# Performance work log

Measured on AMD Instinct MI355X. Metric: run time of the kernel, lower is better.

Reference implementation:

```python
import jax, jax.numpy as jnp
import numpy as np

E = 131072   # total messages
N = 8192     # dim_size (num nodes)
D = 256      # input_dim == hidden_dim (forced by h + m add)


def setup_inputs() -> dict:
    key = jax.random.key(0)
    k1, k2, k3, k4, k5 = jax.random.split(key, 5)
    msg = jax.random.normal(k1, (E, D), dtype=jnp.float32)
    index = jax.random.randint(k2, (E,), 0, N)
    t = jax.random.uniform(k3, (E,), dtype=jnp.float32)
    # torch.nn.Linear(D, D) params (kaiming-uniform-ish scale)
    W = jax.random.normal(k4, (D, D), dtype=jnp.float32) / np.sqrt(D)
    b = (jax.random.normal(k5, (D,), dtype=jnp.float32) * 0.01)
    return {"msg": msg, "index": index, "t": t, "dim_size": N, "W": W, "b": b}


def reference(msg, index, t, dim_size, W, b):
    # Original: for each node, sort its messages by t, then run the linear
    # recurrence h <- W @ (m + h) + b starting from h = 0; nodes with no
    # messages keep h = 0. Vectorized: one global stable sort by (index, t),
    # then a single segmented lax.scan with reset at segment boundaries.
    num_msgs, d = msg.shape
    order = jnp.lexsort((t, index))          # primary key: index, secondary: t
    m_sorted = msg[order]                     # [E, d]
    seg = index[order]                        # [E]

    def step(carry, inp):
        h, prev = carry
        m, s = inp
        h_in = jnp.where(s == prev, h, jnp.zeros_like(h))  # reset at new segment
        h_new = (m + h_in) @ W.T + b
        return (h_new, s), h_new

    init = (jnp.zeros((d,), msg.dtype), jnp.asarray(-1, seg.dtype))
    _, ys = jax.lax.scan(step, init, (m_sorted, seg))      # ys: [E, d]

    # final hidden per node = h at the last message of its segment
    pos = jnp.arange(num_msgs)
    last = jax.ops.segment_max(pos, seg, num_segments=dim_size)
    counts = jax.ops.segment_sum(jnp.ones((num_msgs,), jnp.int32), seg,
                                 num_segments=dim_size)
    gathered = ys[jnp.clip(last, 0, num_msgs - 1)]          # [N, d]
    hidden = jnp.where((counts > 0)[:, None], gathered, jnp.zeros_like(gathered))
    return hidden
```

## Files before the change

### kernel.cpp

```cpp
#include <hip/hip_runtime.h>
#include <hip/hip_bf16.h>

#define E_MSGS 131072
#define N_NODES 8192
#define D_DIM 256
#define XA_STRIDE 264

typedef __bf16 bf16x8 __attribute__((ext_vector_type(8)));
typedef float f32x4 __attribute__((ext_vector_type(4)));

#define BAR() asm volatile("s_waitcnt lgkmcnt(0)\n\ts_barrier" ::: "memory")


__global__ void k_count(const int* __restrict__ index, int* __restrict__ counts) {
    int e = blockIdx.x * blockDim.x + threadIdx.x;
    if (e < E_MSGS) atomicAdd(&counts[index[e]], 1);
}

__global__ void k_prep(const int* __restrict__ counts, int* __restrict__ offsets,
                       int* __restrict__ perm) {
    __shared__ int partial[256];
    __shared__ int hist[256];
    __shared__ int hscan[256];
    __shared__ int hcur[256];
    int tid = threadIdx.x;
    hist[tid] = 0;
    __syncthreads();

    int base = tid * 32;
    int local[32];
    int sum = 0;
#pragma unroll
    for (int i = 0; i < 32; i++) {
        local[i] = sum;
        int c = counts[base + i];
        sum += c;
        atomicAdd(&hist[min(c, 255)], 1);
    }
    partial[tid] = sum;
    __syncthreads();
    for (int off = 1; off < 256; off <<= 1) {
        int v = (tid >= off) ? partial[tid - off] : 0;
        __syncthreads();
        partial[tid] += v;
        __syncthreads();
    }
    int basesum = (tid > 0) ? partial[tid - 1] : 0;
#pragma unroll
    for (int i = 0; i < 32; i++) offsets[base + i] = basesum + local[i];
    if (tid == 255) offsets[N_NODES] = partial[255];

    hscan[tid] = hist[255 - tid];
    __syncthreads();
    for (int off = 1; off < 256; off <<= 1) {
        int v = (tid >= off) ? hscan[tid - off] : 0;
        __syncthreads();
        hscan[tid] += v;
        __syncthreads();
    }
    hcur[tid] = hscan[255 - tid] - hist[tid];
    __syncthreads();
#pragma unroll
    for (int i = 0; i < 32; i++) {
        int n = base + i;
        int c = min(counts[n], 255);
        int pos = atomicAdd(&hcur[c], 1);
        perm[pos] = n;
    }
}

__global__ void k_scatter(const int* __restrict__ index, const int* __restrict__ offsets,
                          int* __restrict__ cursors, int* __restrict__ bucket) {
    int e = blockIdx.x * blockDim.x + threadIdx.x;
    if (e < E_MSGS) {
        int n = index[e];
        int p = offsets[n] + atomicAdd(&cursors[n], 1);
        bucket[p] = e;
    }
}

__global__ void k_sortseg(const float* __restrict__ t, const int* __restrict__ offsets,
                          const int* __restrict__ bucket, int* __restrict__ sorted_id) {
    int wid = (blockIdx.x * 256 + threadIdx.x) >> 6;
    int ln = threadIdx.x & 63;
    int beg = offsets[wid], end = offsets[wid + 1];
    int cnt = end - beg;
    int e = 0; float tv = 0.f;
    if (ln < cnt) { e = bucket[beg + ln]; tv = t[e]; }
    int rank = 0;
    for (int j = 0; j < cnt; j++) {
        float tj = __shfl(tv, j);
        int ej = __shfl(e, j);
        rank += (tj < tv) || (tj == tv && ej < e);
    }
    if (ln < cnt) sorted_id[beg + rank] = e;
}


__launch_bounds__(256, 2)
__global__ void k_gru(const float* __restrict__ msg, const float* __restrict__ W,
                      const float* __restrict__ b, const int* __restrict__ offsets,
                      const int* __restrict__ sorted_id, const int* __restrict__ perm,
                      float* __restrict__ out) {
    __shared__ __bf16 xA[2][16 * XA_STRIDE];

    int tid  = threadIdx.x;
    int wave = tid >> 6;
    int lane = tid & 63;
    int q    = lane >> 4;
    int l    = lane & 15;
    int node0 = blockIdx.x * 16;

    bf16x8 wf[8][4];
#pragma unroll
    for (int t4 = 0; t4 < 4; t4++) {
        const float* wr = W + (64 * wave + 16 * t4 + l) * D_DIM;
#pragma unroll
        for (int c = 0; c < 8; c++) {
            int k0 = 32 * c + 8 * q;
            float4 w0 = *(const float4*)(wr + k0);
            float4 w1 = *(const float4*)(wr + k0 + 4);
            bf16x8 f;
            f[0] = (__bf16)w0.x; f[1] = (__bf16)w0.y; f[2] = (__bf16)w0.z; f[3] = (__bf16)w0.w;
            f[4] = (__bf16)w1.x; f[5] = (__bf16)w1.y; f[6] = (__bf16)w1.z; f[7] = (__bf16)w1.w;
            wf[c][t4] = f;
        }
    }
    float bias[4];
#pragma unroll
    for (int t4 = 0; t4 < 4; t4++) bias[t4] = b[64 * wave + 16 * t4 + l];

    int nodeC[4], off4[4], cnt4[4];
#pragma unroll
    for (int r = 0; r < 4; r++) {
        int n = perm[node0 + 4 * q + r];
        nodeC[r] = n;
        off4[r] = offsets[n];
        cnt4[r] = offsets[n + 1] - off4[r];
    }
    int nfirst = perm[node0];
    int S = offsets[nfirst + 1] - offsets[nfirst];

    float h[4][4];
#pragma unroll
    for (int t4 = 0; t4 < 4; t4++)
#pragma unroll
        for (int r = 0; r < 4; r++) h[t4][r] = 0.f;

    float mvA[4][4], mvB[4][4];
    int sidp[4];
#pragma unroll
    for (int r = 0; r < 4; r++) {
        int sid0 = sorted_id[min(off4[r], E_MSGS - 1)];
        int sid1 = sorted_id[min(off4[r] + 1, E_MSGS - 1)];
        const float* m0 = msg + (long)sid0 * D_DIM;
        const float* m1 = msg + (long)sid1 * D_DIM;
#pragma unroll
        for (int t4 = 0; t4 < 4; t4++) {
            int col = 64 * wave + 16 * t4 + l;
            xA[0][(4 * q + r) * XA_STRIDE + col] = (__bf16)m0[col];
            mvA[r][t4] = m1[col];
        }
        sidp[r] = sorted_id[min(off4[r] + 2, E_MSGS - 1)];
    }
    BAR();

    auto step = [&](int s, float (&cur)[4][4], float (&nxt)[4][4]) {
#pragma unroll
        for (int r = 0; r < 4; r++) {
            const float* mrow = msg + (long)sidp[r] * D_DIM;
#pragma unroll
            for (int t4 = 0; t4 < 4; t4++) nxt[r][t4] = mrow[64 * wave + 16 * t4 + l];
        }
#pragma unroll
        for (int r = 0; r < 4; r++)
            sidp[r] = sorted_id[min(off4[r] + s + 3, E_MSGS - 1)];

        const __bf16* buf = xA[s & 1];
        f32x4 acc[4];
#pragma unroll
        for (int t4 = 0; t4 < 4; t4++) acc[t4] = (f32x4){0.f, 0.f, 0.f, 0.f};
#pragma unroll
        for (int c = 0; c < 8; c++) {
            bf16x8 a = *(const bf16x8*)(buf + l * XA_STRIDE + 32 * c + 8 * q);
#pragma unroll
            for (int t4 = 0; t4 < 4; t4++)
                acc[t4] = __builtin_amdgcn_mfma_f32_16x16x32_bf16(a, wf[c][t4], acc[t4], 0, 0, 0);
        }

        __bf16* nbuf = xA[(s + 1) & 1];
#pragma unroll
        for (int t4 = 0; t4 < 4; t4++) {
#pragma unroll
            for (int r = 0; r < 4; r++) {
                float hn = acc[t4][r] + bias[t4];
                bool valid = s < cnt4[r];
                h[t4][r] = valid ? hn : h[t4][r];
                nbuf[(4 * q + r) * XA_STRIDE + 64 * wave + 16 * t4 + l] =
                    (__bf16)(h[t4][r] + cur[r][t4]);
            }
        }
        BAR();
    };

    int s = 0;
    while (s < S) {
        step(s, mvA, mvB);
        s++;
        if (s >= S) break;
        step(s, mvB, mvA);
        s++;
    }

#pragma unroll
    for (int t4 = 0; t4 < 4; t4++)
#pragma unroll
        for (int r = 0; r < 4; r++)
            out[(long)nodeC[r] * D_DIM + 64 * wave + 16 * t4 + l] = h[t4][r];
}


extern "C" void kernel_launch(void* const* d_in, const int* in_sizes, int n_in,
                              void* d_out, int out_size, void* d_ws, size_t ws_size,
                              hipStream_t stream) {
    const float* msg   = (const float*)d_in[0];
    const int*   index = (const int*)d_in[1];
    const float* t     = (const float*)d_in[2];
    const float* W     = (const float*)d_in[4];
    const float* b     = (const float*)d_in[5];
    float* out = (float*)d_out;

    int* ws = (int*)d_ws;
    int* counts    = ws;
    int* cursors   = ws + 8192;
    int* offsets   = ws + 16384;
    int* perm      = ws + 24584;
    int* bucket    = ws + 32776;
    int* sorted_id = ws + 163848;

    hipMemsetAsync(counts, 0, 16384 * sizeof(int), stream);

    k_count<<<E_MSGS / 256, 256, 0, stream>>>(index, counts);
    k_prep<<<1, 256, 0, stream>>>(counts, offsets, perm);
    k_scatter<<<E_MSGS / 256, 256, 0, stream>>>(index, offsets, cursors, bucket);
    k_sortseg<<<N_NODES * 64 / 256, 256, 0, stream>>>(t, offsets, bucket, sorted_id);
    k_gru<<<N_NODES / 16, 256, 0, stream>>>(msg, W, b, offsets, sorted_id, perm, out);
}
```

Baseline: 256.7 us.

## Fuse per-node time sort into GRU kernel and drop degree-sorted node permutation

The per-segment timestamp sort moves into the recurrence kernel. Each block ranks its 16 nodes' messages with wave shuffles into a shared-memory id table, which removes the separate sort kernel and its global sorted_id round trip. The single-block prefix scan is rewritten as a 1024-thread shuffle scan that also zeroes the scatter cursors, so the memset shrinks. Nodes are now processed in natural order instead of the count-sorted permutation, which drops the histogram work. The cost is that each block runs for the longest segment among its 16 nodes, and segments are capped at 64 messages.

```diff
diff --git a/kernel.cpp b/kernel.cpp
--- a/kernel.cpp
+++ b/kernel.cpp
@@ -17,56 +17,42 @@
     if (e < E_MSGS) atomicAdd(&counts[index[e]], 1);
 }
 
-__global__ void k_prep(const int* __restrict__ counts, int* __restrict__ offsets,
-                       int* __restrict__ perm) {
-    __shared__ int partial[256];
-    __shared__ int hist[256];
-    __shared__ int hscan[256];
-    __shared__ int hcur[256];
-    int tid = threadIdx.x;
-    hist[tid] = 0;
+__global__ void k_scan(const int* __restrict__ counts, int* __restrict__ offsets,
+                       int* __restrict__ cursors) {
+    __shared__ int wsum[16], wpre[16];
+    int tid = threadIdx.x, lane = tid & 63, wave = tid >> 6;
+    int base = tid * 8;
+    int4 c0 = *(const int4*)(counts + base);
+    int4 c1 = *(const int4*)(counts + base + 4);
+    int v[8] = {c0.x, c0.y, c0.z, c0.w, c1.x, c1.y, c1.z, c1.w};
+    int loc[8], sum = 0;
+#pragma unroll
+    for (int i = 0; i < 8; i++) { loc[i] = sum; sum += v[i]; }
+    int incl = sum;
+#pragma unroll
+    for (int d = 1; d < 64; d <<= 1) {
+        int u = __shfl_up(incl, d);
+        if (lane >= d) incl += u;
+    }
+    if (lane == 63) wsum[wave] = incl;
     __syncthreads();
-
-    int base = tid * 32;
-    int local[32];
-    int sum = 0;
-#pragma unroll
-    for (int i = 0; i < 32; i++) {
-        local[i] = sum;
-        int c = counts[base + i];
-        sum += c;
-        atomicAdd(&hist[min(c, 255)], 1);
-    }
-    partial[tid] = sum;
+    if (tid < 16) {
+        int w = wsum[tid], p = w;
+#pragma unroll
+        for (int d = 1; d < 16; d <<= 1) {
+            int u = __shfl_up(p, d);
+            if (tid >= d) p += u;
+        }
+        wpre[tid] = p - w;
+    }
     __syncthreads();
-    for (int off = 1; off < 256; off <<= 1) {
-        int v = (tid >= off) ? partial[tid - off] : 0;
-        __syncthreads();
-        partial[tid] += v;
-        __syncthreads();
-    }
-    int basesum = (tid > 0) ? partial[tid - 1] : 0;
-#pragma unroll
-    for (int i = 0; i < 32; i++) offsets[base + i] = basesum + local[i];
-    if (tid == 255) offsets[N_NODES] = partial[255];
-
-    hscan[tid] = hist[255 - tid];
-    __syncthreads();
-    for (int off = 1; off < 256; off <<= 1) {
-        int v = (tid >= off) ? hscan[tid - off] : 0;
-        __syncthreads();
-        hscan[tid] += v;
-        __syncthreads();
-    }
-    hcur[tid] = hscan[255 - tid] - hist[tid];
-    __syncthreads();
-#pragma unroll
-    for (int i = 0; i < 32; i++) {
-        int n = base + i;
-        int c = min(counts[n], 255);
-        int pos = atomicAdd(&hcur[c], 1);
-        perm[pos] = n;
-    }
+    int ebase = wpre[wave] + incl - sum;
+#pragma unroll
+    for (int i = 0; i < 8; i++) offsets[base + i] = ebase + loc[i];
+    int4 z = {0, 0, 0, 0};
+    *(int4*)(cursors + base) = z;
+    *(int4*)(cursors + base + 4) = z;
+    if (tid == 0) offsets[N_NODES] = E_MSGS;
 }
 
 __global__ void k_scatter(const int* __restrict__ index, const int* __restrict__ offsets,
@@ -79,36 +65,52 @@
     }
 }
 
-__global__ void k_sortseg(const float* __restrict__ t, const int* __restrict__ offsets,
-                          const int* __restrict__ bucket, int* __restrict__ sorted_id) {
-    int wid = (blockIdx.x * 256 + threadIdx.x) >> 6;
-    int ln = threadIdx.x & 63;
-    int beg = offsets[wid], end = offsets[wid + 1];
-    int cnt = end - beg;
-    int e = 0; float tv = 0.f;
-    if (ln < cnt) { e = bucket[beg + ln]; tv = t[e]; }
-    int rank = 0;
-    for (int j = 0; j < cnt; j++) {
-        float tj = __shfl(tv, j);
-        int ej = __shfl(e, j);
-        rank += (tj < tv) || (tj == tv && ej < e);
-    }
-    if (ln < cnt) sorted_id[beg + rank] = e;
-}
-
+
+#define GRU_STEP(SS, CUR, NXT)                                                 \
+    {                                                                          \
+        _Pragma("unroll") for (int r = 0; r < 4; r++) {                        \
+            const float* mrow = msg + (long)sidR[r] * D_DIM;                   \
+            _Pragma("unroll") for (int t4 = 0; t4 < 4; t4++)                   \
+                NXT[r][t4] = mrow[64 * wave + 16 * t4 + l];                     \
+        }                                                                      \
+        {                                                                      \
+            int row = (SS) + 3 < 64 ? (SS) + 3 : 63;                           \
+            int4 sr = *(const int4*)&sid[row][4 * q];                          \
+            sidR[0] = sr.x; sidR[1] = sr.y; sidR[2] = sr.z; sidR[3] = sr.w;    \
+        }                                                                      \
+        const __bf16* buf = xA[(SS) & 1];                                      \
+        f32x4 acc[4];                                                          \
+        _Pragma("unroll") for (int t4 = 0; t4 < 4; t4++)                       \
+            acc[t4] = (f32x4){0.f, 0.f, 0.f, 0.f};                             \
+        _Pragma("unroll") for (int c = 0; c < 8; c++) {                        \
+            bf16x8 a = *(const bf16x8*)(buf + l * XA_STRIDE + 32 * c + 8 * q); \
+            _Pragma("unroll") for (int t4 = 0; t4 < 4; t4++)                   \
+                acc[t4] = __builtin_amdgcn_mfma_f32_16x16x32_bf16(             \
+                    a, wf[c][t4], acc[t4], 0, 0, 0);                           \
+        }                                                                      \
+        __bf16* nbuf = xA[((SS) + 1) & 1];                                     \
+        _Pragma("unroll") for (int t4 = 0; t4 < 4; t4++) {                     \
+            _Pragma("unroll") for (int r = 0; r < 4; r++) {                    \
+                float hn = acc[t4][r] + bias[t4];                              \
+                bool valid = (SS) < cnt4[r];                                   \
+                h[t4][r] = valid ? hn : h[t4][r];                              \
+                nbuf[(4 * q + r) * XA_STRIDE + 64 * wave + 16 * t4 + l] =      \
+                    (__bf16)(h[t4][r] + CUR[r][t4]);                           \
+            }                                                                  \
+        }                                                                      \
+        BAR();                                                                 \
+    }
 
 __launch_bounds__(256, 2)
-__global__ void k_gru(const float* __restrict__ msg, const float* __restrict__ W,
+__global__ void k_gru(const float* __restrict__ msg, const float* __restrict__ t,
+                      const int* __restrict__ bucket, const float* __restrict__ W,
                       const float* __restrict__ b, const int* __restrict__ offsets,
-                      const int* __restrict__ sorted_id, const int* __restrict__ perm,
                       float* __restrict__ out) {
     __shared__ __bf16 xA[2][16 * XA_STRIDE];
-
-    int tid  = threadIdx.x;
-    int wave = tid >> 6;
-    int lane = tid & 63;
-    int q    = lane >> 4;
-    int l    = lane & 15;
+    __shared__ int sid[64][16];
+
+    int tid = threadIdx.x;
+    int wave = tid >> 6, lane = tid & 63, q = lane >> 4, l = lane & 15;
     int node0 = blockIdx.x * 16;
 
     bf16x8 wf[8][4];
@@ -130,16 +132,33 @@
 #pragma unroll
     for (int t4 = 0; t4 < 4; t4++) bias[t4] = b[64 * wave + 16 * t4 + l];
 
-    int nodeC[4], off4[4], cnt4[4];
+    int off4[4], cnt4[4];
 #pragma unroll
     for (int r = 0; r < 4; r++) {
-        int n = perm[node0 + 4 * q + r];
-        nodeC[r] = n;
-        off4[r] = offsets[n];
-        cnt4[r] = offsets[n + 1] - off4[r];
-    }
-    int nfirst = perm[node0];
-    int S = offsets[nfirst + 1] - offsets[nfirst];
+        off4[r] = offsets[node0 + 4 * q + r];
+        cnt4[r] = offsets[node0 + 4 * q + r + 1] - off4[r];
+    }
+    int mc = max(max(cnt4[0], cnt4[1]), max(cnt4[2], cnt4[3]));
+    mc = max(mc, __shfl_xor(mc, 16));
+    mc = max(mc, __shfl_xor(mc, 32));
+    int S = mc;
+
+    for (int i = 0; i < 4; i++) {
+        int j = 4 * wave + i;
+        int beg = offsets[node0 + j];
+        int cnt = min(offsets[node0 + j + 1] - beg, 64);
+        sid[lane][j] = 0;
+        int e = 0; float tv = 0.f;
+        if (lane < cnt) { e = bucket[beg + lane]; tv = t[e]; }
+        int rank = 0;
+        for (int j2 = 0; j2 < cnt; j2++) {
+            float tj = __shfl(tv, j2);
+            int ej = __shfl(e, j2);
+            rank += (tj < tv) || (tj == tv && ej < e);
+        }
+        if (lane < cnt) sid[rank][j] = e;
+    }
+    BAR();
 
     float h[4][4];
 #pragma unroll
@@ -148,75 +167,38 @@
         for (int r = 0; r < 4; r++) h[t4][r] = 0.f;
 
     float mvA[4][4], mvB[4][4];
-    int sidp[4];
+    int sidR[4];
+    int4 sr0 = *(const int4*)&sid[0][4 * q];
+    int4 sr1 = *(const int4*)&sid[1][4 * q];
+    int4 sr2 = *(const int4*)&sid[2][4 * q];
+    int s0[4] = {sr0.x, sr0.y, sr0.z, sr0.w};
+    int s1[4] = {sr1.x, sr1.y, sr1.z, sr1.w};
+    sidR[0] = sr2.x; sidR[1] = sr2.y; sidR[2] = sr2.z; sidR[3] = sr2.w;
 #pragma unroll
     for (int r = 0; r < 4; r++) {
-        int sid0 = sorted_id[min(off4[r], E_MSGS - 1)];
-        int sid1 = sorted_id[min(off4[r] + 1, E_MSGS - 1)];
-        const float* m0 = msg + (long)sid0 * D_DIM;
-        const float* m1 = msg + (long)sid1 * D_DIM;
+        const float* m0 = msg + (long)s0[r] * D_DIM;
+        const float* m1 = msg + (long)s1[r] * D_DIM;
 #pragma unroll
         for (int t4 = 0; t4 < 4; t4++) {
             int col = 64 * wave + 16 * t4 + l;
             xA[0][(4 * q + r) * XA_STRIDE + col] = (__bf16)m0[col];
             mvA[r][t4] = m1[col];
         }
-        sidp[r] = sorted_id[min(off4[r] + 2, E_MSGS - 1)];
     }
     BAR();
-
-    auto step = [&](int s, float (&cur)[4][4], float (&nxt)[4][4]) {
-#pragma unroll
-        for (int r = 0; r < 4; r++) {
-            const float* mrow = msg + (long)sidp[r] * D_DIM;
-#pragma unroll
-            for (int t4 = 0; t4 < 4; t4++) nxt[r][t4] = mrow[64 * wave + 16 * t4 + l];
-        }
-#pragma unroll
-        for (int r = 0; r < 4; r++)
-            sidp[r] = sorted_id[min(off4[r] + s + 3, E_MSGS - 1)];
-
-        const __bf16* buf = xA[s & 1];
-        f32x4 acc[4];
-#pragma unroll
-        for (int t4 = 0; t4 < 4; t4++) acc[t4] = (f32x4){0.f, 0.f, 0.f, 0.f};
-#pragma unroll
-        for (int c = 0; c < 8; c++) {
-            bf16x8 a = *(const bf16x8*)(buf + l * XA_STRIDE + 32 * c + 8 * q);
-#pragma unroll
-            for (int t4 = 0; t4 < 4; t4++)
-                acc[t4] = __builtin_amdgcn_mfma_f32_16x16x32_bf16(a, wf[c][t4], acc[t4], 0, 0, 0);
-        }
-
-        __bf16* nbuf = xA[(s + 1) & 1];
-#pragma unroll
-        for (int t4 = 0; t4 < 4; t4++) {
-#pragma unroll
-            for (int r = 0; r < 4; r++) {
-                float hn = acc[t4][r] + bias[t4];
-                bool valid = s < cnt4[r];
-                h[t4][r] = valid ? hn : h[t4][r];
-                nbuf[(4 * q + r) * XA_STRIDE + 64 * wave + 16 * t4 + l] =
-                    (__bf16)(h[t4][r] + cur[r][t4]);
-            }
-        }
-        BAR();
-    };
 
     int s = 0;
     while (s < S) {
-        step(s, mvA, mvB);
-        s++;
+        GRU_STEP(s, mvA, mvB); s++;
         if (s >= S) break;
-        step(s, mvB, mvA);
-        s++;
+        GRU_STEP(s, mvB, mvA); s++;
     }
 
 #pragma unroll
     for (int t4 = 0; t4 < 4; t4++)
 #pragma unroll
         for (int r = 0; r < 4; r++)
-            out[(long)nodeC[r] * D_DIM + 64 * wave + 16 * t4 + l] = h[t4][r];
+            out[(long)(node0 + 4 * q + r) * D_DIM + 64 * wave + 16 * t4 + l] = h[t4][r];
 }
 
 
@@ -231,18 +213,15 @@
     float* out = (float*)d_out;
 
     int* ws = (int*)d_ws;
-    int* counts    = ws;
-    int* cursors   = ws + 8192;
-    int* offsets   = ws + 16384;
-    int* perm      = ws + 24584;
-    int* bucket    = ws + 32776;
-    int* sorted_id = ws + 163848;
-
-    hipMemsetAsync(counts, 0, 16384 * sizeof(int), stream);
+    int* counts  = ws;
+    int* cursors = ws + 8192;
+    int* offsets = ws + 16384;
+    int* bucket  = ws + 24584;
+
+    hipMemsetAsync(counts, 0, 8192 * sizeof(int), stream);
 
     k_count<<<E_MSGS / 256, 256, 0, stream>>>(index, counts);
-    k_prep<<<1, 256, 0, stream>>>(counts, offsets, perm);
+    k_scan<<<1, 1024, 0, stream>>>(counts, offsets, cursors);
     k_scatter<<<E_MSGS / 256, 256, 0, stream>>>(index, offsets, cursors, bucket);
-    k_sortseg<<<N_NODES * 64 / 256, 256, 0, stream>>>(t, offsets, bucket, sorted_id);
-    k_gru<<<N_NODES / 16, 256, 0, stream>>>(msg, W, b, offsets, sorted_id, perm, out);
-}
+    k_gru<<<N_NODES / 16, 256, 0, stream>>>(msg, t, bucket, W, b, offsets, out);
+}
```

After: 266.3 us. +3.8%, slower.

## Use padded per-node buckets instead of CSR offsets and split GRU across eight waves

Applied to the files above, without the earlier changes.

Replaces the count, prefix-scan and scatter pipeline with a single atomic scatter into fixed 64-slot per-node buckets. This removes one kernel and the single-block offset scan, and the per-segment sort is done in place. The recurrence kernel now runs 512 threads per block, so each wave owns 32 output columns instead of 64, halving per-wave MFMA and register work per step. The trade-offs are a larger workspace memset, and any node with more than 64 messages is silently truncated. The old sort already could only handle up to 64 messages per node.

```diff
diff --git a/kernel.cpp b/kernel.cpp
--- a/kernel.cpp
+++ b/kernel.cpp
@@ -12,95 +12,62 @@
 #define BAR() asm volatile("s_waitcnt lgkmcnt(0)\n\ts_barrier" ::: "memory")
 
 
-__global__ void k_count(const int* __restrict__ index, int* __restrict__ counts) {
+__global__ void k_scatter(const int* __restrict__ index, int* __restrict__ cursors,
+                          int* __restrict__ pad) {
     int e = blockIdx.x * blockDim.x + threadIdx.x;
-    if (e < E_MSGS) atomicAdd(&counts[index[e]], 1);
-}
-
-__global__ void k_prep(const int* __restrict__ counts, int* __restrict__ offsets,
-                       int* __restrict__ perm) {
-    __shared__ int partial[256];
-    __shared__ int hist[256];
-    __shared__ int hscan[256];
-    __shared__ int hcur[256];
+    int n = index[e];
+    int p = atomicAdd(&cursors[n], 1);
+    if (p < 64) pad[(n << 6) + p] = e;
+}
+
+__global__ void k_perm(const int* __restrict__ counts, int* __restrict__ perm) {
+    __shared__ int hist[65];
+    __shared__ int hcur[65];
     int tid = threadIdx.x;
-    hist[tid] = 0;
+    if (tid < 65) hist[tid] = 0;
     __syncthreads();
-
-    int base = tid * 32;
-    int local[32];
-    int sum = 0;
+    int myc[32];
 #pragma unroll
     for (int i = 0; i < 32; i++) {
-        local[i] = sum;
-        int c = counts[base + i];
-        sum += c;
-        atomicAdd(&hist[min(c, 255)], 1);
-    }
-    partial[tid] = sum;
+        int c = min(counts[tid * 32 + i], 64);
+        myc[i] = c;
+        atomicAdd(&hist[c], 1);
+    }
     __syncthreads();
-    for (int off = 1; off < 256; off <<= 1) {
-        int v = (tid >= off) ? partial[tid - off] : 0;
-        __syncthreads();
-        partial[tid] += v;
-        __syncthreads();
-    }
-    int basesum = (tid > 0) ? partial[tid - 1] : 0;
-#pragma unroll
-    for (int i = 0; i < 32; i++) offsets[base + i] = basesum + local[i];
-    if (tid == 255) offsets[N_NODES] = partial[255];
-
-    hscan[tid] = hist[255 - tid];
+    if (tid == 0) {
+        int run = 0;
+        for (int c = 64; c >= 0; c--) { hcur[c] = run; run += hist[c]; }
+    }
     __syncthreads();
-    for (int off = 1; off < 256; off <<= 1) {
-        int v = (tid >= off) ? hscan[tid - off] : 0;
-        __syncthreads();
-        hscan[tid] += v;
-        __syncthreads();
-    }
-    hcur[tid] = hscan[255 - tid] - hist[tid];
-    __syncthreads();
 #pragma unroll
     for (int i = 0; i < 32; i++) {
-        int n = base + i;
-        int c = min(counts[n], 255);
-        int pos = atomicAdd(&hcur[c], 1);
-        perm[pos] = n;
-    }
-}
-
-__global__ void k_scatter(const int* __restrict__ index, const int* __restrict__ offsets,
-                          int* __restrict__ cursors, int* __restrict__ bucket) {
-    int e = blockIdx.x * blockDim.x + threadIdx.x;
-    if (e < E_MSGS) {
-        int n = index[e];
-        int p = offsets[n] + atomicAdd(&cursors[n], 1);
-        bucket[p] = e;
-    }
-}
-
-__global__ void k_sortseg(const float* __restrict__ t, const int* __restrict__ offsets,
-                          const int* __restrict__ bucket, int* __restrict__ sorted_id) {
+        int pos = atomicAdd(&hcur[myc[i]], 1);
+        perm[pos] = tid * 32 + i;
+    }
+}
+
+__global__ void k_sortseg(const float* __restrict__ t, const int* __restrict__ counts,
+                          int* __restrict__ pad) {
     int wid = (blockIdx.x * 256 + threadIdx.x) >> 6;
     int ln = threadIdx.x & 63;
-    int beg = offsets[wid], end = offsets[wid + 1];
-    int cnt = end - beg;
+    int cnt = min(counts[wid], 64);
+    int base = wid << 6;
     int e = 0; float tv = 0.f;
-    if (ln < cnt) { e = bucket[beg + ln]; tv = t[e]; }
+    if (ln < cnt) { e = pad[base + ln]; tv = t[e]; }
     int rank = 0;
     for (int j = 0; j < cnt; j++) {
         float tj = __shfl(tv, j);
         int ej = __shfl(e, j);
         rank += (tj < tv) || (tj == tv && ej < e);
     }
-    if (ln < cnt) sorted_id[beg + rank] = e;
-}
-
-
-__launch_bounds__(256, 2)
+    if (ln < cnt) pad[base + rank] = e;
+}
+
+
+__launch_bounds__(512, 4)
 __global__ void k_gru(const float* __restrict__ msg, const float* __restrict__ W,
-                      const float* __restrict__ b, const int* __restrict__ offsets,
-                      const int* __restrict__ sorted_id, const int* __restrict__ perm,
+                      const float* __restrict__ b, const int* __restrict__ counts,
+                      const int* __restrict__ spad, const int* __restrict__ perm,
                       float* __restrict__ out) {
     __shared__ __bf16 xA[2][16 * XA_STRIDE];
 
@@ -111,10 +78,10 @@
     int l    = lane & 15;
     int node0 = blockIdx.x * 16;
 
-    bf16x8 wf[8][4];
-#pragma unroll
-    for (int t4 = 0; t4 < 4; t4++) {
-        const float* wr = W + (64 * wave + 16 * t4 + l) * D_DIM;
+    bf16x8 wf[8][2];
+#pragma unroll
+    for (int t4 = 0; t4 < 2; t4++) {
+        const float* wr = W + (32 * wave + 16 * t4 + l) * D_DIM;
 #pragma unroll
         for (int c = 0; c < 8; c++) {
             int k0 = 32 * c + 8 * q;
@@ -126,77 +93,75 @@
             wf[c][t4] = f;
         }
     }
-    float bias[4];
-#pragma unroll
-    for (int t4 = 0; t4 < 4; t4++) bias[t4] = b[64 * wave + 16 * t4 + l];
-
-    int nodeC[4], off4[4], cnt4[4];
+    float bias[2];
+#pragma unroll
+    for (int t4 = 0; t4 < 2; t4++) bias[t4] = b[32 * wave + 16 * t4 + l];
+
+    int base4[4], cnt4[4];
 #pragma unroll
     for (int r = 0; r < 4; r++) {
         int n = perm[node0 + 4 * q + r];
-        nodeC[r] = n;
-        off4[r] = offsets[n];
-        cnt4[r] = offsets[n + 1] - off4[r];
-    }
-    int nfirst = perm[node0];
-    int S = offsets[nfirst + 1] - offsets[nfirst];
-
-    float h[4][4];
-#pragma unroll
-    for (int t4 = 0; t4 < 4; t4++)
+        base4[r] = n << 6;
+        cnt4[r] = min(counts[n], 64);
+    }
+    int S = min(counts[perm[node0]], 64);
+
+    float h[2][4];
+#pragma unroll
+    for (int t4 = 0; t4 < 2; t4++)
 #pragma unroll
         for (int r = 0; r < 4; r++) h[t4][r] = 0.f;
 
-    float mvA[4][4], mvB[4][4];
+    float mvA[4][2], mvB[4][2];
     int sidp[4];
 #pragma unroll
     for (int r = 0; r < 4; r++) {
-        int sid0 = sorted_id[min(off4[r], E_MSGS - 1)];
-        int sid1 = sorted_id[min(off4[r] + 1, E_MSGS - 1)];
-        const float* m0 = msg + (long)sid0 * D_DIM;
-        const float* m1 = msg + (long)sid1 * D_DIM;
-#pragma unroll
-        for (int t4 = 0; t4 < 4; t4++) {
-            int col = 64 * wave + 16 * t4 + l;
+        int s0 = spad[base4[r]];
+        int s1 = spad[base4[r] + 1];
+        const float* m0 = msg + (long)s0 * D_DIM;
+        const float* m1 = msg + (long)s1 * D_DIM;
+#pragma unroll
+        for (int t4 = 0; t4 < 2; t4++) {
+            int col = 32 * wave + 16 * t4 + l;
             xA[0][(4 * q + r) * XA_STRIDE + col] = (__bf16)m0[col];
             mvA[r][t4] = m1[col];
         }
-        sidp[r] = sorted_id[min(off4[r] + 2, E_MSGS - 1)];
+        sidp[r] = spad[base4[r] + 2];
     }
     BAR();
 
-    auto step = [&](int s, float (&cur)[4][4], float (&nxt)[4][4]) {
+    auto step = [&](int s, float (&cur)[4][2], float (&nxt)[4][2]) {
 #pragma unroll
         for (int r = 0; r < 4; r++) {
             const float* mrow = msg + (long)sidp[r] * D_DIM;
 #pragma unroll
-            for (int t4 = 0; t4 < 4; t4++) nxt[r][t4] = mrow[64 * wave + 16 * t4 + l];
+            for (int t4 = 0; t4 < 2; t4++) nxt[r][t4] = mrow[32 * wave + 16 * t4 + l];
         }
 #pragma unroll
         for (int r = 0; r < 4; r++)
-            sidp[r] = sorted_id[min(off4[r] + s + 3, E_MSGS - 1)];
+            sidp[r] = spad[base4[r] + min(s + 3, 63)];
 
         const __bf16* buf = xA[s & 1];
-        f32x4 acc[4];
-#pragma unroll
-        for (int t4 = 0; t4 < 4; t4++) acc[t4] = (f32x4){0.f, 0.f, 0.f, 0.f};
+        f32x4 acc[2];
+#pragma unroll
+        for (int t4 = 0; t4 < 2; t4++) acc[t4] = (f32x4){0.f, 0.f, 0.f, 0.f};
 #pragma unroll
         for (int c = 0; c < 8; c++) {
             bf16x8 a = *(const bf16x8*)(buf + l * XA_STRIDE + 32 * c + 8 * q);
 #pragma unroll
-            for (int t4 = 0; t4 < 4; t4++)
+            for (int t4 = 0; t4 < 2; t4++)
                 acc[t4] = __builtin_amdgcn_mfma_f32_16x16x32_bf16(a, wf[c][t4], acc[t4], 0, 0, 0);
         }
 
         __bf16* nbuf = xA[(s + 1) & 1];
 #pragma unroll
-        for (int t4 = 0; t4 < 4; t4++) {
+        for (int t4 = 0; t4 < 2; t4++) {
 #pragma unroll
             for (int r = 0; r < 4; r++) {
                 float hn = acc[t4][r] + bias[t4];
                 bool valid = s < cnt4[r];
                 h[t4][r] = valid ? hn : h[t4][r];
-                nbuf[(4 * q + r) * XA_STRIDE + 64 * wave + 16 * t4 + l] =
+                nbuf[(4 * q + r) * XA_STRIDE + 32 * wave + 16 * t4 + l] =
                     (__bf16)(h[t4][r] + cur[r][t4]);
             }
         }
@@ -213,10 +178,12 @@
     }
 
 #pragma unroll
-    for (int t4 = 0; t4 < 4; t4++)
-#pragma unroll
-        for (int r = 0; r < 4; r++)
-            out[(long)nodeC[r] * D_DIM + 64 * wave + 16 * t4 + l] = h[t4][r];
+    for (int r = 0; r < 4; r++) {
+        int n = perm[node0 + 4 * q + r];
+#pragma unroll
+        for (int t4 = 0; t4 < 2; t4++)
+            out[(long)n * D_DIM + 32 * wave + 16 * t4 + l] = h[t4][r];
+    }
 }
 
 
@@ -231,18 +198,14 @@
     float* out = (float*)d_out;
 
     int* ws = (int*)d_ws;
-    int* counts    = ws;
-    int* cursors   = ws + 8192;
-    int* offsets   = ws + 16384;
-    int* perm      = ws + 24584;
-    int* bucket    = ws + 32776;
-    int* sorted_id = ws + 163848;
-
-    hipMemsetAsync(counts, 0, 16384 * sizeof(int), stream);
-
-    k_count<<<E_MSGS / 256, 256, 0, stream>>>(index, counts);
-    k_prep<<<1, 256, 0, stream>>>(counts, offsets, perm);
-    k_scatter<<<E_MSGS / 256, 256, 0, stream>>>(index, offsets, cursors, bucket);
-    k_sortseg<<<N_NODES * 64 / 256, 256, 0, stream>>>(t, offsets, bucket, sorted_id);
-    k_gru<<<N_NODES / 16, 256, 0, stream>>>(msg, W, b, offsets, sorted_id, perm, out);
-}
+    int* cursors = ws;
+    int* pad     = ws + 8192;
+    int* perm    = ws + 8192 + 8192 * 64;
+
+    hipMemsetAsync(cursors, 0, (8192 + 8192 * 64) * sizeof(int), stream);
+
+    k_scatter<<<E_MSGS / 256, 256, 0, stream>>>(index, cursors, pad);
+    k_perm<<<1, 256, 0, stream>>>(cursors, perm);
+    k_sortseg<<<N_NODES * 64 / 256, 256, 0, stream>>>(t, cursors, pad);
+    k_gru<<<N_NODES / 16, 512, 0, stream>>>(msg, W, b, cursors, pad, perm, out);
+}
```

After: 250.4 us. -2.4%, faster.
